# Kernel optimization log

Measured on AMD Instinct MI355X. Metric: run time of the kernel, lower is better.

The kernel has to match this reference:

```python
import jax, jax.numpy as jnp
import numpy as np

NNODE = 500000       # nodes -> 2*NNODE global DOFs
NELEM = 500000       # elements, 8 DOF each (2D quad)
NDOF = 2 * NNODE


def setup_inputs() -> dict:
    key = jax.random.key(0)
    k1, k2, k3, k4 = jax.random.split(key, 4)
    u = jax.random.normal(k1, (NDOF,), dtype=jnp.float32)
    weight1 = jax.random.normal(k2, (NDOF,), dtype=jnp.float32)
    bc_idx = jnp.arange(NDOF, dtype=jnp.int64)  # free-DOF indices (all free)
    # elemental DOF map: 8 global DOF indices per element (irregular)
    edof = jax.random.randint(k3, (NELEM, 8), 0, NDOF, dtype=jnp.int64)
    # per-element 8x8 stiffness matrices
    stiffness = jax.random.normal(k4, (NELEM, 8, 8), dtype=jnp.float32)
    return {"u": u, "weight1": weight1, "bc_idx": bc_idx,
            "edof": edof, "stiffness": stiffness}


def reference(u, weight1, bc_idx, edof, stiffness):
    # u1 = zeros; u1[bc_idx] = weight1 * u[bc_idx]
    u1 = jnp.zeros_like(u).at[bc_idx].set(weight1 * u[bc_idx])
    # gather elemental DOF values: [E, 8]
    ue = u1[edof]
    # per-element stiffness matvec: [E, 8]
    fe = jnp.einsum('eij,ej->ei', stiffness, ue)
    # scatter-add assembly into global force vector
    F = jnp.zeros_like(u).at[edof.reshape(-1)].add(fe.reshape(-1))
    return F
```

## Files before the change

### kernel.cpp

```cpp
#include <hip/hip_runtime.h>

typedef float vfloat4 __attribute__((ext_vector_type(4)));
typedef int   vint4   __attribute__((ext_vector_type(4)));

#define BSHIFT 12
#define BSIZE  4096
#define G1     512
#define TPB    256

__global__ void scatter_u1_kernel(const float* __restrict__ u,
                                  const float* __restrict__ w1,
                                  const int* __restrict__ bc,
                                  float* __restrict__ u1, int n) {
    int k = blockIdx.x * blockDim.x + threadIdx.x;
    if (k < n) {
        int idx = bc[k];
        u1[idx] = w1[k] * u[idx];
    }
}

__global__ void compute_fe_kernel(const float* __restrict__ u1,
                                  const int* __restrict__ edof,
                                  const float* __restrict__ stiff,
                                  float* __restrict__ febuf, int nelem) {
    int t = blockIdx.x * blockDim.x + threadIdx.x;
    int e = t >> 3;
    if (e >= nelem) return;
    int i = t & 7;

    int idx = __builtin_nontemporal_load(edof + t);
    float ue = u1[idx];

    const vfloat4* Kr = (const vfloat4*)(stiff + (size_t)e * 64 + (size_t)i * 8);
    vfloat4 k0 = __builtin_nontemporal_load(Kr);
    vfloat4 k1 = __builtin_nontemporal_load(Kr + 1);

    float fe;
    fe  = k0.x * __shfl(ue, 0, 8);
    fe += k0.y * __shfl(ue, 1, 8);
    fe += k0.z * __shfl(ue, 2, 8);
    fe += k0.w * __shfl(ue, 3, 8);
    fe += k1.x * __shfl(ue, 4, 8);
    fe += k1.y * __shfl(ue, 5, 8);
    fe += k1.z * __shfl(ue, 6, 8);
    fe += k1.w * __shfl(ue, 7, 8);

    __builtin_nontemporal_store(fe, febuf + t);
}

__global__ void hist_kernel(const int* __restrict__ edof,
                            int* __restrict__ cnt,
                            int total, int nb, int chunk) {
    __shared__ int h[256];
    int wg = blockIdx.x;
    if (threadIdx.x < nb) h[threadIdx.x] = 0;
    __syncthreads();
    int k0 = wg * chunk;
    int k1 = min(k0 + chunk, total);
    for (int k = k0 + threadIdx.x * 4; k < k1; k += TPB * 4) {
        vint4 v = __builtin_nontemporal_load((const vint4*)(edof + k));
        atomicAdd(&h[v.x >> BSHIFT], 1);
        atomicAdd(&h[v.y >> BSHIFT], 1);
        atomicAdd(&h[v.z >> BSHIFT], 1);
        atomicAdd(&h[v.w >> BSHIFT], 1);
    }
    __syncthreads();
    if (threadIdx.x < nb) cnt[threadIdx.x * G1 + wg] = h[threadIdx.x];
}

__global__ void scan_bucket_kernel(const int* __restrict__ cnt,
                                   int* __restrict__ wgoff,
                                   int* __restrict__ btot) {
    int b = blockIdx.x;
    int lane = threadIdx.x;
    const int per = G1 / 64;
    int v[per];
    int s = 0;
    for (int j = 0; j < per; ++j) { v[j] = cnt[b * G1 + lane * per + j]; s += v[j]; }
    int incl = s;
    for (int off = 1; off < 64; off <<= 1) {
        int n = __shfl_up(incl, off, 64);
        if (lane >= off) incl += n;
    }
    int run = incl - s;
    for (int j = 0; j < per; ++j) { wgoff[b * G1 + lane * per + j] = run; run += v[j]; }
    if (lane == 63) btot[b] = incl;
}

__global__ void scan_total_kernel(const int* __restrict__ btot,
                                  int* __restrict__ bstart, int nb) {
    int lane = threadIdx.x;
    int v[4];
    int s = 0;
    for (int j = 0; j < 4; ++j) {
        int i = lane * 4 + j;
        v[j] = (i < nb) ? btot[i] : 0;
        s += v[j];
    }
    int incl = s;
    for (int off = 1; off < 64; off <<= 1) {
        int n = __shfl_up(incl, off, 64);
        if (lane >= off) incl += n;
    }
    int run = incl - s;
    for (int j = 0; j < 4; ++j) {
        int i = lane * 4 + j;
        if (i < nb) bstart[i] = run;
        run += v[j];
    }
    if (lane == 63) bstart[nb] = incl;
}

__global__ void scatter_pairs_kernel(const int* __restrict__ edof,
                                     const float* __restrict__ febuf,
                                     const int* __restrict__ wgoff,
                                     const int* __restrict__ bstart,
                                     unsigned int* __restrict__ pairs,
                                     int total, int nb, int chunk) {
    __shared__ int base[256];
    int wg = blockIdx.x;
    if (threadIdx.x < nb)
        base[threadIdx.x] = bstart[threadIdx.x] + wgoff[threadIdx.x * G1 + wg];
    __syncthreads();
    int k0 = wg * chunk;
    int k1 = min(k0 + chunk, total);
    for (int k = k0 + threadIdx.x * 4; k < k1; k += TPB * 4) {
        vint4   idx = __builtin_nontemporal_load((const vint4*)(edof + k));
        vfloat4 fev = __builtin_nontemporal_load((const vfloat4*)(febuf + k));
        int   ids[4] = {idx.x, idx.y, idx.z, idx.w};
        float fes[4] = {fev.x, fev.y, fev.z, fev.w};
        #pragma unroll
        for (int j = 0; j < 4; ++j) {
            int id = ids[j];
            int b = id >> BSHIFT;
            int pos = atomicAdd(&base[b], 1);
            unsigned short hu = __builtin_bit_cast(unsigned short, (_Float16)fes[j]);
            pairs[pos] = ((unsigned)(id & (BSIZE - 1)) << 16) | (unsigned)hu;
        }
    }
}

__global__ void bucket_reduce_kernel(const unsigned int* __restrict__ pairs,
                                     const int* __restrict__ bstart,
                                     float* __restrict__ F, int ndof) {
    __shared__ float acc[BSIZE];
    int b = blockIdx.x;
    for (int j = threadIdx.x; j < BSIZE; j += TPB) acc[j] = 0.0f;
    __syncthreads();
    int k0 = bstart[b], k1 = bstart[b + 1];
    for (int k = k0 + threadIdx.x; k < k1; k += TPB) {
        unsigned p = pairs[k];
        float fe = (float)__builtin_bit_cast(_Float16, (unsigned short)(p & 0xffffu));
        atomicAdd(&acc[p >> 16], fe);
    }
    __syncthreads();
    int gbase = b << BSHIFT;
    for (int j = threadIdx.x; j < BSIZE; j += TPB) {
        int g = gbase + j;
        if (g < ndof) F[g] = acc[j];
    }
}

__global__ void elem_assemble_kernel(const float* __restrict__ u1,
                                     const int* __restrict__ edof,
                                     const float* __restrict__ stiff,
                                     float* __restrict__ F, int nelem) {
    int t = blockIdx.x * blockDim.x + threadIdx.x;
    int e = t >> 3;
    if (e >= nelem) return;
    int i = t & 7;
    int idx = __builtin_nontemporal_load(edof + t);
    float ue = u1[idx];
    const vfloat4* Kr = (const vfloat4*)(stiff + (size_t)e * 64 + (size_t)i * 8);
    vfloat4 k0 = __builtin_nontemporal_load(Kr);
    vfloat4 k1 = __builtin_nontemporal_load(Kr + 1);
    float fe;
    fe  = k0.x * __shfl(ue, 0, 8);
    fe += k0.y * __shfl(ue, 1, 8);
    fe += k0.z * __shfl(ue, 2, 8);
    fe += k0.w * __shfl(ue, 3, 8);
    fe += k1.x * __shfl(ue, 4, 8);
    fe += k1.y * __shfl(ue, 5, 8);
    fe += k1.z * __shfl(ue, 6, 8);
    fe += k1.w * __shfl(ue, 7, 8);
    unsafeAtomicAdd(&F[idx], fe);
}

extern "C" void kernel_launch(void* const* d_in, const int* in_sizes, int n_in,
                              void* d_out, int out_size, void* d_ws, size_t ws_size,
                              hipStream_t stream) {
    const float* u     = (const float*)d_in[0];
    const float* w1    = (const float*)d_in[1];
    const int*   bc    = (const int*)d_in[2];
    const int*   edof  = (const int*)d_in[3];
    const float* stiff = (const float*)d_in[4];
    float* F = (float*)d_out;

    int ndof  = in_sizes[0];
    int nbc   = in_sizes[2];
    int total = in_sizes[3];
    int nelem = total / 8;
    int nb    = (ndof + BSIZE - 1) >> BSHIFT;

    char* w = (char*)d_ws;
    size_t o = 0;
    auto take = [&](size_t nbytes) -> char* {
        char* p = w + o;
        o += (nbytes + 255) & ~(size_t)255;
        return p;
    };
    float* u1    = (float*)take((size_t)ndof * 4);
    float* febuf = (float*)take((size_t)total * 4);
    unsigned int* pairs = (unsigned int*)take((size_t)total * 4);
    int* cnt    = (int*)take((size_t)nb * G1 * 4);
    int* wgoff  = (int*)take((size_t)nb * G1 * 4);
    int* btot   = (int*)take((size_t)nb * 4);
    int* bstart = (int*)take((size_t)(nb + 1) * 4);

    (void)hipMemsetAsync(u1, 0, (size_t)ndof * sizeof(float), stream);
    scatter_u1_kernel<<<(nbc + TPB - 1) / TPB, TPB, 0, stream>>>(u, w1, bc, u1, nbc);

    if (o <= ws_size && nb <= 256 && total % 8 == 0) {
        int chunk = (((total + G1 - 1) / G1) + 1023) & ~1023;
        hist_kernel<<<G1, TPB, 0, stream>>>(edof, cnt, total, nb, chunk);
        scan_bucket_kernel<<<nb, 64, 0, stream>>>(cnt, wgoff, btot);
        scan_total_kernel<<<1, 64, 0, stream>>>(btot, bstart, nb);
        compute_fe_kernel<<<(total + TPB - 1) / TPB, TPB, 0, stream>>>(
            u1, edof, stiff, febuf, nelem);
        scatter_pairs_kernel<<<G1, TPB, 0, stream>>>(
            edof, febuf, wgoff, bstart, pairs, total, nb, chunk);
        bucket_reduce_kernel<<<nb, TPB, 0, stream>>>(pairs, bstart, F, ndof);
    } else {
        (void)hipMemsetAsync(F, 0, (size_t)ndof * sizeof(float), stream);
        elem_assemble_kernel<<<(total + TPB - 1) / TPB, TPB, 0, stream>>>(
            u1, edof, stiff, F, nelem);
    }
}
```

Before: 301.1 us.

## Fuse element matvec into histogram pass and store fe as fp16

Merges the per-element stiffness matvec into the bucket histogram kernel, so edof is read once for both and one launch is removed. The fe buffer now holds fp16 values, halving its write and read traffic; the fp16 conversion moves out of the scatter-pairs kernel. The bucket reduce kernel also runs with 512 threads per block instead of 256. The fused kernel runs only 512 blocks with a per-thread strided loop, so it may expose less parallelism and latency hiding than the old one-thread-per-entry matvec launch.

```diff
diff --git a/kernel.cpp b/kernel.cpp
--- a/kernel.cpp
+++ b/kernel.cpp
@@ -1,7 +1,8 @@
 #include <hip/hip_runtime.h>
 
-typedef float vfloat4 __attribute__((ext_vector_type(4)));
-typedef int   vint4   __attribute__((ext_vector_type(4)));
+typedef float          vfloat4  __attribute__((ext_vector_type(4)));
+typedef int            vint4    __attribute__((ext_vector_type(4)));
+typedef unsigned short vushort4 __attribute__((ext_vector_type(4)));
 
 #define BSHIFT 12
 #define BSIZE  4096
@@ -19,50 +20,41 @@
     }
 }
 
-__global__ void compute_fe_kernel(const float* __restrict__ u1,
-                                  const int* __restrict__ edof,
-                                  const float* __restrict__ stiff,
-                                  float* __restrict__ febuf, int nelem) {
-    int t = blockIdx.x * blockDim.x + threadIdx.x;
-    int e = t >> 3;
-    if (e >= nelem) return;
-    int i = t & 7;
-
-    int idx = __builtin_nontemporal_load(edof + t);
-    float ue = u1[idx];
-
-    const vfloat4* Kr = (const vfloat4*)(stiff + (size_t)e * 64 + (size_t)i * 8);
-    vfloat4 k0 = __builtin_nontemporal_load(Kr);
-    vfloat4 k1 = __builtin_nontemporal_load(Kr + 1);
-
-    float fe;
-    fe  = k0.x * __shfl(ue, 0, 8);
-    fe += k0.y * __shfl(ue, 1, 8);
-    fe += k0.z * __shfl(ue, 2, 8);
-    fe += k0.w * __shfl(ue, 3, 8);
-    fe += k1.x * __shfl(ue, 4, 8);
-    fe += k1.y * __shfl(ue, 5, 8);
-    fe += k1.z * __shfl(ue, 6, 8);
-    fe += k1.w * __shfl(ue, 7, 8);
-
-    __builtin_nontemporal_store(fe, febuf + t);
-}
-
-__global__ void hist_kernel(const int* __restrict__ edof,
-                            int* __restrict__ cnt,
-                            int total, int nb, int chunk) {
+__global__ void compute_fe_hist_kernel(const float* __restrict__ u1,
+                                       const int* __restrict__ edof,
+                                       const float* __restrict__ stiff,
+                                       unsigned short* __restrict__ febuf16,
+                                       int* __restrict__ cnt,
+                                       int total, int nb, int chunk) {
     __shared__ int h[256];
     int wg = blockIdx.x;
     if (threadIdx.x < nb) h[threadIdx.x] = 0;
     __syncthreads();
     int k0 = wg * chunk;
     int k1 = min(k0 + chunk, total);
-    for (int k = k0 + threadIdx.x * 4; k < k1; k += TPB * 4) {
-        vint4 v = __builtin_nontemporal_load((const vint4*)(edof + k));
-        atomicAdd(&h[v.x >> BSHIFT], 1);
-        atomicAdd(&h[v.y >> BSHIFT], 1);
-        atomicAdd(&h[v.z >> BSHIFT], 1);
-        atomicAdd(&h[v.w >> BSHIFT], 1);
+    for (int k = k0 + threadIdx.x; k < k1; k += TPB) {
+        int e = k >> 3;
+        int i = k & 7;
+        int idx = __builtin_nontemporal_load(edof + k);
+        float ue = u1[idx];
+
+        const vfloat4* Kr = (const vfloat4*)(stiff + (size_t)e * 64 + (size_t)i * 8);
+        vfloat4 ka = __builtin_nontemporal_load(Kr);
+        vfloat4 kb = __builtin_nontemporal_load(Kr + 1);
+
+        float fe;
+        fe  = ka.x * __shfl(ue, 0, 8);
+        fe += ka.y * __shfl(ue, 1, 8);
+        fe += ka.z * __shfl(ue, 2, 8);
+        fe += ka.w * __shfl(ue, 3, 8);
+        fe += kb.x * __shfl(ue, 4, 8);
+        fe += kb.y * __shfl(ue, 5, 8);
+        fe += kb.z * __shfl(ue, 6, 8);
+        fe += kb.w * __shfl(ue, 7, 8);
+
+        unsigned short hu = __builtin_bit_cast(unsigned short, (_Float16)fe);
+        __builtin_nontemporal_store(hu, febuf16 + k);
+        atomicAdd(&h[idx >> BSHIFT], 1);
     }
     __syncthreads();
     if (threadIdx.x < nb) cnt[threadIdx.x * G1 + wg] = h[threadIdx.x];
@@ -112,7 +104,7 @@
 }
 
 __global__ void scatter_pairs_kernel(const int* __restrict__ edof,
-                                     const float* __restrict__ febuf,
+                                     const unsigned short* __restrict__ febuf16,
                                      const int* __restrict__ wgoff,
                                      const int* __restrict__ bstart,
                                      unsigned int* __restrict__ pairs,
@@ -125,17 +117,16 @@
     int k0 = wg * chunk;
     int k1 = min(k0 + chunk, total);
     for (int k = k0 + threadIdx.x * 4; k < k1; k += TPB * 4) {
-        vint4   idx = __builtin_nontemporal_load((const vint4*)(edof + k));
-        vfloat4 fev = __builtin_nontemporal_load((const vfloat4*)(febuf + k));
-        int   ids[4] = {idx.x, idx.y, idx.z, idx.w};
-        float fes[4] = {fev.x, fev.y, fev.z, fev.w};
+        vint4    idx = __builtin_nontemporal_load((const vint4*)(edof + k));
+        vushort4 hv  = __builtin_nontemporal_load((const vushort4*)(febuf16 + k));
+        int      ids[4] = {idx.x, idx.y, idx.z, idx.w};
+        unsigned hus[4] = {hv.x, hv.y, hv.z, hv.w};
         #pragma unroll
         for (int j = 0; j < 4; ++j) {
             int id = ids[j];
             int b = id >> BSHIFT;
             int pos = atomicAdd(&base[b], 1);
-            unsigned short hu = __builtin_bit_cast(unsigned short, (_Float16)fes[j]);
-            pairs[pos] = ((unsigned)(id & (BSIZE - 1)) << 16) | (unsigned)hu;
+            pairs[pos] = ((unsigned)(id & (BSIZE - 1)) << 16) | hus[j];
         }
     }
 }
@@ -145,17 +136,17 @@
                                      float* __restrict__ F, int ndof) {
     __shared__ float acc[BSIZE];
     int b = blockIdx.x;
-    for (int j = threadIdx.x; j < BSIZE; j += TPB) acc[j] = 0.0f;
+    for (int j = threadIdx.x; j < BSIZE; j += 512) acc[j] = 0.0f;
     __syncthreads();
     int k0 = bstart[b], k1 = bstart[b + 1];
-    for (int k = k0 + threadIdx.x; k < k1; k += TPB) {
+    for (int k = k0 + threadIdx.x; k < k1; k += 512) {
         unsigned p = pairs[k];
         float fe = (float)__builtin_bit_cast(_Float16, (unsigned short)(p & 0xffffu));
         atomicAdd(&acc[p >> 16], fe);
     }
     __syncthreads();
     int gbase = b << BSHIFT;
-    for (int j = threadIdx.x; j < BSIZE; j += TPB) {
+    for (int j = threadIdx.x; j < BSIZE; j += 512) {
         int g = gbase + j;
         if (g < ndof) F[g] = acc[j];
     }
@@ -209,8 +200,8 @@
         o += (nbytes + 255) & ~(size_t)255;
         return p;
     };
-    float* u1    = (float*)take((size_t)ndof * 4);
-    float* febuf = (float*)take((size_t)total * 4);
+    float* u1 = (float*)take((size_t)ndof * 4);
+    unsigned short* febuf16 = (unsigned short*)take((size_t)total * 2);
     unsigned int* pairs = (unsigned int*)take((size_t)total * 4);
     int* cnt    = (int*)take((size_t)nb * G1 * 4);
     int* wgoff  = (int*)take((size_t)nb * G1 * 4);
@@ -222,14 +213,13 @@
 
     if (o <= ws_size && nb <= 256 && total % 8 == 0) {
         int chunk = (((total + G1 - 1) / G1) + 1023) & ~1023;
-        hist_kernel<<<G1, TPB, 0, stream>>>(edof, cnt, total, nb, chunk);
+        compute_fe_hist_kernel<<<G1, TPB, 0, stream>>>(
+            u1, edof, stiff, febuf16, cnt, total, nb, chunk);
         scan_bucket_kernel<<<nb, 64, 0, stream>>>(cnt, wgoff, btot);
         scan_total_kernel<<<1, 64, 0, stream>>>(btot, bstart, nb);
-        compute_fe_kernel<<<(total + TPB - 1) / TPB, TPB, 0, stream>>>(
-            u1, edof, stiff, febuf, nelem);
         scatter_pairs_kernel<<<G1, TPB, 0, stream>>>(
-            edof, febuf, wgoff, bstart, pairs, total, nb, chunk);
-        bucket_reduce_kernel<<<nb, TPB, 0, stream>>>(pairs, bstart, F, ndof);
+            edof, febuf16, wgoff, bstart, pairs, total, nb, chunk);
+        bucket_reduce_kernel<<<nb, 512, 0, stream>>>(pairs, bstart, F, ndof);
     } else {
         (void)hipMemsetAsync(F, 0, (size_t)ndof * sizeof(float), stream);
         elem_assemble_kernel<<<(total + TPB - 1) / TPB, TPB, 0, stream>>>(
```

After: 299.9 us. About the same (-0.4%).
